# Optimization experiments

Hardware: AMD Instinct MI355X
Metric: run time of the kernel (lower is better)

Reference implementation:

```python
import jax, jax.numpy as jnp
import numpy as np

B, NSM, NLG = 64, 400, 196
SM, LG = 512, 1024
D, H, DH = 4, 16, 64
INNER = H * DH
EPS = 1e-5


def setup_inputs() -> dict:
    key = jax.random.key(0)
    ks = iter(jax.random.split(key, 40))
    def rn(shape, s=0.02):
        return jax.random.normal(next(ks), shape, jnp.float32) * s
    inp = {
        "sm_tokens": rn((B, NSM + 1, SM), 1.0),
        "lg_tokens": rn((B, NLG + 1, LG), 1.0),
    }
    def branch(p, din, dout):
        inp[p + "_pin_w"] = rn((D, din, dout))
        inp[p + "_pin_b"] = jnp.zeros((D, dout), jnp.float32)
        inp[p + "_ng"] = jnp.ones((D, dout), jnp.float32)
        inp[p + "_nb"] = jnp.zeros((D, dout), jnp.float32)
        inp[p + "_wq"] = rn((D, dout, INNER))
        inp[p + "_wkv"] = rn((D, dout, 2 * INNER))
        inp[p + "_wo"] = rn((D, INNER, dout))
        inp[p + "_wob"] = jnp.zeros((D, dout), jnp.float32)
        inp[p + "_pout_w"] = rn((D, dout, din))
        inp[p + "_pout_b"] = jnp.zeros((D, din), jnp.float32)
    branch("a", SM, LG)   # sm_attend_lg: project sm->lg, attention in lg_dim
    branch("b", LG, SM)   # lg_attend_sm: project lg->sm, attention in sm_dim
    return inp


def _attn(cls_tok, ctx, ng, nb, wq, wkv, wo, wob):
    # cls_tok: [B,1,dim]; ctx: [B,S,dim]. Matches lucidrains cross_vit Attention:
    # LayerNorm(x) first; kv context = concat(normed_x, context); context NOT normed.
    scale = DH ** -0.5
    mu = cls_tok.mean(-1, keepdims=True)
    var = ((cls_tok - mu) ** 2).mean(-1, keepdims=True)
    xn = (cls_tok - mu) * jax.lax.rsqrt(var + EPS) * ng + nb
    c = jnp.concatenate([xn, ctx], axis=1)             # kv_include_self=True
    q = (xn @ wq).reshape(B, 1, H, DH)
    k, v = jnp.split(c @ wkv, 2, axis=-1)
    k = k.reshape(B, -1, H, DH)
    v = v.reshape(B, -1, H, DH)
    s = jnp.einsum('bqhd,bkhd->bhqk', q, k) * scale     # [B,H,1,S+1]
    p = jax.nn.softmax(s, axis=-1)
    o = jnp.einsum('bhqk,bkhd->bqhd', p, v).reshape(B, 1, INNER)
    return o @ wo + wob


def _forward(sm_tokens, lg_tokens,
             a_pin_w, a_pin_b, a_ng, a_nb, a_wq, a_wkv, a_wo, a_wob, a_pout_w, a_pout_b,
             b_pin_w, b_pin_b, b_ng, b_nb, b_wq, b_wkv, b_wo, b_wob, b_pout_w, b_pout_b):
    sm_cls, sm_patch = sm_tokens[:, :1], sm_tokens[:, 1:]
    lg_cls, lg_patch = lg_tokens[:, :1], lg_tokens[:, 1:]
    for i in range(D):
        x = sm_cls @ a_pin_w[i] + a_pin_b[i]
        x = _attn(x, lg_patch, a_ng[i], a_nb[i], a_wq[i], a_wkv[i], a_wo[i], a_wob[i])
        sm_cls = x @ a_pout_w[i] + a_pout_b[i] + sm_cls
        y = lg_cls @ b_pin_w[i] + b_pin_b[i]
        y = _attn(y, sm_patch, b_ng[i], b_nb[i], b_wq[i], b_wkv[i], b_wo[i], b_wob[i])
        lg_cls = y @ b_pout_w[i] + b_pout_b[i] + lg_cls
    sm_out = jnp.concatenate([sm_cls, sm_patch], axis=1)
    lg_out = jnp.concatenate([lg_cls, lg_patch], axis=1)
    return sm_out, lg_out


def reference(sm_tokens, lg_tokens,
              a_pin_w, a_pin_b, a_ng, a_nb, a_wq, a_wkv, a_wo, a_wob, a_pout_w, a_pout_b,
              b_pin_w, b_pin_b, b_ng, b_nb, b_wq, b_wkv, b_wo, b_wob, b_pout_w, b_pout_b):
    return _forward(sm_tokens, lg_tokens,
                    a_pin_w, a_pin_b, a_ng, a_nb, a_wq, a_wkv, a_wo, a_wob, a_pout_w, a_pout_b,
                    b_pin_w, b_pin_b, b_ng, b_nb, b_wq, b_wkv, b_wo, b_wob, b_pout_w, b_pout_b)
```

## Files before the change

### kernel.cpp

```cpp
#include <hip/hip_runtime.h>
#include <hip/hip_bf16.h>
#include <math.h>

#define B_     64
#define NSM_   400
#define NLG_   196
#define SM_    512
#define LG_    1024
#define H_     16
#define DH_    64
#define INNER_ 1024
#define SSTR   424
#define PSTR   424

typedef __attribute__((ext_vector_type(8))) short bf16x8;
typedef __attribute__((ext_vector_type(8))) unsigned short u16x8;
typedef __attribute__((ext_vector_type(4))) float f32x4;

__device__ __forceinline__ unsigned short f2b(float f) {
  unsigned u = __float_as_uint(f);
  u = u + 0x7FFFu + ((u >> 16) & 1u);
  return (unsigned short)(u >> 16);
}
__device__ __forceinline__ f32x4 zero4() {
  f32x4 a; a[0] = 0.f; a[1] = 0.f; a[2] = 0.f; a[3] = 0.f; return a;
}


struct CC2 { const float* tok; float* out; unsigned short* abf; float* cls;
             unsigned short* clsb; int Np1, nf4, shift, tot4; };
struct WTDesc { const float* src; unsigned short* dst; unsigned short* dst2; int K, N; };
struct WTArgs { WTDesc d[10]; int cum[11]; };
__global__ __launch_bounds__(256) void setup1(CC2 ca, CC2 cb, WTArgs W, int nw) {
  __shared__ unsigned short tile[64][68];
  const int tid = threadIdx.x;
  if ((int)blockIdx.x < nw) {
    int bx = blockIdx.x, di = 0;
    while (bx >= W.cum[di + 1]) di++;
    int local = bx - W.cum[di];
    WTDesc g = W.d[di];
    int tn = g.N >> 6;
    int tpl = tn * (g.K >> 6);
    int layer = local / tpl, rem = local % tpl;
    int kt = (rem / tn) * 64, nt = (rem % tn) * 64;
    const float* wp = g.src + (size_t)layer * g.K * g.N;
    unsigned short* op = g.dst + (size_t)layer * g.K * g.N;
    unsigned short* d2 = (g.dst2 && nt < 1024)
                             ? g.dst2 + (size_t)layer * g.K * 1024 : nullptr;
#pragma unroll
    for (int p = 0; p < 4; p++) {
      int r = (tid >> 4) + p * 16;
      int c = (tid & 15) * 4;
      const f32x4 v = __builtin_nontemporal_load(
          (const f32x4*)&wp[(size_t)(kt + r) * g.N + nt + c]);
      ushort4 w4;
      w4.x = f2b(v.x); w4.y = f2b(v.y); w4.z = f2b(v.z); w4.w = f2b(v.w);
      *(ushort4*)&tile[r][c] = w4;
      if (d2) *(ushort4*)&d2[(size_t)(kt + r) * 1024 + nt + c] = w4;
    }
    __syncthreads();
    const int r2 = tid >> 2, cseg = tid & 3;
    u16x8 v0, v1;
#pragma unroll
    for (int i = 0; i < 8; i++) v0[i] = tile[cseg * 16 + i][r2];
#pragma unroll
    for (int i = 0; i < 8; i++) v1[i] = tile[cseg * 16 + 8 + i][r2];
    unsigned short* orow = &op[(size_t)(nt + r2) * g.K + kt + cseg * 16];
    *(u16x8*)&orow[0] = v0;
    *(u16x8*)&orow[8] = v1;
  } else {
    const int nblk = gridDim.x - nw;
    const int total = ca.tot4 + cb.tot4;
    for (int i = ((int)blockIdx.x - nw) * 256 + tid; i < total; i += nblk * 256) {
      CC2 g; int idx;
      if (i < ca.tot4) { g = ca; idx = i; } else { g = cb; idx = i - ca.tot4; }
      int rowg = idx >> g.shift, t = idx & ((1 << g.shift) - 1);
      int bb = rowg / g.Np1, row = rowg - bb * g.Np1;
      const f32x4 v = __builtin_nontemporal_load(&((const f32x4*)g.tok)[idx]);
      __builtin_nontemporal_store(v, &((f32x4*)g.out)[idx]);
      ushort4 w2; w2.x = f2b(v.x); w2.y = f2b(v.y); w2.z = f2b(v.z); w2.w = f2b(v.w);
      if (row > 0) {
        ((ushort4*)g.abf)[(size_t)(bb * (g.Np1 - 1) + row - 1) * g.nf4 + t] = w2;
      } else {
        ((f32x4*)g.cls)[(size_t)bb * g.nf4 + t] = v;
        ((ushort4*)g.clsb)[(size_t)bb * g.nf4 + t] = w2;
      }
    }
  }
}

struct TXArgs { const unsigned short* xbf; unsigned short* xT; int Nctx, dout, xstride, nx, ny, nblk; };
__global__ __launch_bounds__(256) void setup2(TXArgs ta, TXArgs tb) {
  __shared__ unsigned short tile[64][68];
  TXArgs g; int bx = blockIdx.x;
  if (bx < ta.nblk) { g = ta; } else { g = tb; bx -= ta.nblk; }
  int cx = bx % g.nx; int rem = bx / g.nx;
  int jy = rem % g.ny; int b = rem / g.ny;
  int jt = jy * 64, ct = cx * 64;
  const int tid = threadIdx.x;
#pragma unroll
  for (int p = 0; p < 4; p++) {
    int row = (tid >> 4) + p * 16;
    int c = (tid & 15) * 4;
    int j = jt + row;
    ushort4 v;
    if (j < g.Nctx) v = *(const ushort4*)&g.xbf[((size_t)b * g.Nctx + j) * g.dout + ct + c];
    else { v.x = 0; v.y = 0; v.z = 0; v.w = 0; }
    *(ushort4*)&tile[row][c] = v;
  }
  __syncthreads();
  const int r2 = tid >> 2, jseg = tid & 3;
  if (jt + jseg * 16 < g.xstride) {
    u16x8 v0, v1;
#pragma unroll
    for (int i = 0; i < 8; i++) v0[i] = tile[jseg * 16 + i][r2];
#pragma unroll
    for (int i = 0; i < 8; i++) v1[i] = tile[jseg * 16 + 8 + i][r2];
    unsigned short* orow = &g.xT[((size_t)b * g.dout + ct + r2) * g.xstride + jt + jseg * 16];
    *(u16x8*)&orow[0] = v0;
    *(u16x8*)&orow[8] = v1;
  }
}

struct SGDesc {
  const unsigned short* A; const unsigned short* WT; const float* bias;
  float* Cf; unsigned short* Cbf; const float* Rf;
  int K, N;
  float* outF; int ostride;
};
struct SGArgs { SGDesc d[4]; int cum[5]; int nd; };
__global__ __launch_bounds__(256) void sg_wide(SGArgs W) {
  int bx = blockIdx.x, di = 0;
  while (di < W.nd - 1 && bx >= W.cum[di + 1]) di++;
  SGDesc g = W.d[di];
  const int n0 = (bx - W.cum[di]) * 16;
  const int tid = threadIdx.x;
  const int lane = tid & 63, mt = tid >> 6;
  const int r16 = lane & 15, kv8 = (lane >> 4) * 8;
  f32x4 acc0 = zero4(), acc1 = zero4();
  const unsigned short* wp = &g.WT[(size_t)(n0 + r16) * g.K + kv8];
  const unsigned short* ap = &g.A[(size_t)(mt * 16 + r16) * g.K + kv8];
  const int K = g.K;
#pragma unroll 2
  for (int k0 = 0; k0 < K; k0 += 64) {
    acc0 = __builtin_amdgcn_mfma_f32_16x16x32_bf16(*(const bf16x8*)&ap[k0],
                                                   *(const bf16x8*)&wp[k0], acc0, 0, 0, 0);
    acc1 = __builtin_amdgcn_mfma_f32_16x16x32_bf16(*(const bf16x8*)&ap[k0 + 32],
                                                   *(const bf16x8*)&wp[k0 + 32], acc1, 0, 0, 0);
  }
  const int rbase = (lane >> 4) * 4;
#pragma unroll
  for (int rr = 0; rr < 4; rr++) {
    int r = mt * 16 + rbase + rr, c = n0 + r16;
    float v = acc0[rr] + acc1[rr];
    if (g.bias) v += g.bias[c];
    if (g.Rf) v += g.Rf[(size_t)r * g.N + c];
    if (g.Cf)  g.Cf[(size_t)r * g.N + c] = v;
    if (g.Cbf) g.Cbf[(size_t)r * g.N + c] = f2b(v);
    if (g.outF) g.outF[(size_t)r * g.ostride + c] = v;
  }
}

struct LNArgs { const float* x; unsigned short* xnb; const float* ng; const float* nb; int dim; };
__global__ __launch_bounds__(256) void ln2(LNArgs la, LNArgs lb) {
  LNArgs g = ((int)blockIdx.x < 64) ? la : lb;
  int b = blockIdx.x & 63, t = threadIdx.x;
  __shared__ float rs[4], rq[4], bc[2];
  const float* xp = g.x + (size_t)b * g.dim;
  float s = 0.f, sq = 0.f;
  for (int c = t; c < g.dim; c += 256) {
    float v = xp[c];
    s += v; sq += v * v;
  }
#pragma unroll
  for (int off = 32; off >= 1; off >>= 1) {
    s += __shfl_down(s, off);
    sq += __shfl_down(sq, off);
  }
  int w = t >> 6;
  if ((t & 63) == 0) { rs[w] = s; rq[w] = sq; }
  __syncthreads();
  if (t == 0) {
    float ts = rs[0] + rs[1] + rs[2] + rs[3];
    float tq = rq[0] + rq[1] + rq[2] + rq[3];
    float mu = ts / g.dim;
    float var = tq / g.dim - mu * mu;
    bc[0] = mu; bc[1] = rsqrtf(var + 1e-5f);
  }
  __syncthreads();
  float mu = bc[0], r = bc[1];
  for (int c = t; c < g.dim; c += 256)
    g.xnb[(size_t)b * g.dim + c] = f2b((xp[c] - mu) * r * g.ng[c] + g.nb[c]);
}

struct QTArgs { const unsigned short* qb16; const unsigned short* wkvnb;
                unsigned short* qt; int dout, ntiles, nblk; };
__global__ __launch_bounds__(256) void qtilde3(QTArgs ga, QTArgs gb) {
  QTArgs g; int bx = blockIdx.x;
  if (bx < ga.nblk) g = ga; else { g = gb; bx -= ga.nblk; }
  const int h = bx / g.ntiles, nt = bx - h * g.ntiles;
  const int n0 = nt * 16;
  const int tid = threadIdx.x, lane = tid & 63, mt = tid >> 6;
  const int r16 = lane & 15, kv8 = (lane >> 4) * 8;
  const unsigned short* ap = g.qb16 + (size_t)(mt * 16 + r16) * INNER_ + h * 64 + kv8;
  const unsigned short* bp = g.wkvnb + (size_t)(n0 + r16) * 1024 + h * 64 + kv8;
  f32x4 acc0 = zero4(), acc1 = zero4();
  acc0 = __builtin_amdgcn_mfma_f32_16x16x32_bf16(*(const bf16x8*)&ap[0],
                                                 *(const bf16x8*)&bp[0], acc0, 0, 0, 0);
  acc1 = __builtin_amdgcn_mfma_f32_16x16x32_bf16(*(const bf16x8*)&ap[32],
                                                 *(const bf16x8*)&bp[32], acc1, 0, 0, 0);
  const int rbase = (lane >> 4) * 4;
#pragma unroll
  for (int rr = 0; rr < 4; rr++) {
    int b = mt * 16 + rbase + rr;
    g.qt[((size_t)b * 16 + h) * g.dout + n0 + r16] = f2b(acc0[rr] + acc1[rr]);
  }
}

struct SArgs { const unsigned short* qt; const unsigned short* xbf; float* S;
               int dout, Nctx, ntj, nbj, nblk; };
__global__ __launch_bounds__(256) void s_gemm(SArgs ga, SArgs gb) {
  SArgs g; int bx;
  if ((int)blockIdx.x < ga.nblk) { g = ga; bx = blockIdx.x; }
  else { g = gb; bx = blockIdx.x - ga.nblk; }
  const int b = bx / g.nbj, jq = bx - b * g.nbj;
  const int tid = threadIdx.x, lane = tid & 63, w = tid >> 6;
  const int jt = jq * 4 + w;
  if (jt >= g.ntj) return;
  const int r16 = lane & 15, kv8 = (lane >> 4) * 8;
  const unsigned short* ap = g.qt + ((size_t)b * 16 + r16) * g.dout + kv8;
  const unsigned short* bp = g.xbf + ((size_t)b * g.Nctx + jt * 16 + r16) * g.dout + kv8;
  f32x4 acc0 = zero4(), acc1 = zero4();
  const int K = g.dout;
#pragma unroll 2
  for (int k0 = 0; k0 < K; k0 += 64) {
    acc0 = __builtin_amdgcn_mfma_f32_16x16x32_bf16(*(const bf16x8*)&ap[k0],
                                                   *(const bf16x8*)&bp[k0], acc0, 0, 0, 0);
    acc1 = __builtin_amdgcn_mfma_f32_16x16x32_bf16(*(const bf16x8*)&ap[k0 + 32],
                                                   *(const bf16x8*)&bp[k0 + 32], acc1, 0, 0, 0);
  }
  const int rbase = (lane >> 4) * 4;
#pragma unroll
  for (int rr = 0; rr < 4; rr++)
    g.S[((size_t)b * 16 + rbase + rr) * SSTR + jt * 16 + r16] = acc0[rr] + acc1[rr];
}

struct SMArgs { const float* S; const float* qb; const float* kvc;
                unsigned short* p; float* pcls; int Nctx, Npad; };
__global__ __launch_bounds__(256) void softmax_p2(SMArgs ga, SMArgs gb) {
  SMArgs g = blockIdx.z ? gb : ga;
  const int h = blockIdx.x, b = blockIdx.y;
  const int t = threadIdx.x;
  __shared__ float red[4], bc;
  float sc = 0.f;
  if (t < 64) sc = g.qb[(size_t)b * INNER_ + h * 64 + t] * g.kvc[(size_t)b * 2048 + h * 64 + t];
#pragma unroll
  for (int o = 32; o >= 1; o >>= 1) sc += __shfl_down(sc, o);
  if (t == 0) bc = sc * 0.125f;
  __syncthreads();
  const float scls = bc;
  const float* Sp = g.S + ((size_t)b * 16 + h) * SSTR;

  float sraw[2] = {-1e30f, -1e30f};
#pragma unroll
  for (int u2 = 0; u2 < 2; u2++) {
    int j = t + u2 * 256;
    if (j < g.Nctx) sraw[u2] = Sp[j] * 0.125f;
  }
  float mx = fmaxf(fmaxf(sraw[0], sraw[1]), scls);
#pragma unroll
  for (int o = 32; o >= 1; o >>= 1) mx = fmaxf(mx, __shfl_down(mx, o));
  if ((t & 63) == 0) red[t >> 6] = mx;
  __syncthreads();
  mx = fmaxf(fmaxf(red[0], red[1]), fmaxf(red[2], red[3]));
  __syncthreads();

  float e0 = (t < g.Nctx) ? expf(sraw[0] - mx) : 0.f;
  float e1 = (t + 256 < g.Nctx) ? expf(sraw[1] - mx) : 0.f;
  float ecls = expf(scls - mx);
  float ls = e0 + e1;
#pragma unroll
  for (int o = 32; o >= 1; o >>= 1) ls += __shfl_down(ls, o);
  if ((t & 63) == 0) red[t >> 6] = ls;
  __syncthreads();
  const float denom = red[0] + red[1] + red[2] + red[3] + ecls;
  const float inv = 1.f / denom;

  unsigned short* pp = g.p + ((size_t)b * 16 + h) * PSTR;
  if (t < g.Nctx) pp[t] = f2b(e0 * inv);
  if (t + 256 < g.Nctx) pp[t + 256] = f2b(e1 * inv);
  for (int j = g.Nctx + t; j < g.Npad; j += 256) pp[j] = 0;
  if (t == 0) g.pcls[b * 16 + h] = ecls * inv;
}

struct UG { const unsigned short* p; const unsigned short* xT; unsigned short* u;
            int dout, Npad, xstride, ntx; };
__global__ __launch_bounds__(256) void ugemm2(UG ga, UG gb) {
  UG g; int bx = blockIdx.x;
  if (bx < ga.ntx) g = ga; else { g = gb; bx -= ga.ntx; }
  const int b = blockIdx.y;
  const int tid = threadIdx.x, lane = tid & 63, w = tid >> 6;
  const int c0 = bx * 64 + w * 16;
  const int r16 = lane & 15, kv8 = (lane >> 4) * 8, rbase = (lane >> 4) * 4;
  const unsigned short* ap = g.p + ((size_t)b * 16 + r16) * PSTR + kv8;
  const unsigned short* bp = g.xT + ((size_t)b * g.dout + c0 + r16) * g.xstride + kv8;
  f32x4 acc0 = zero4(), acc1 = zero4();
  const int Kp = g.Npad;
  int k0 = 0;
  for (; k0 + 64 <= Kp; k0 += 64) {
    acc0 = __builtin_amdgcn_mfma_f32_16x16x32_bf16(*(const bf16x8*)&ap[k0],
                                                   *(const bf16x8*)&bp[k0], acc0, 0, 0, 0);
    acc1 = __builtin_amdgcn_mfma_f32_16x16x32_bf16(*(const bf16x8*)&ap[k0 + 32],
                                                   *(const bf16x8*)&bp[k0 + 32], acc1, 0, 0, 0);
  }
  if (k0 < Kp)
    acc0 = __builtin_amdgcn_mfma_f32_16x16x32_bf16(*(const bf16x8*)&ap[k0],
                                                   *(const bf16x8*)&bp[k0], acc0, 0, 0, 0);
#pragma unroll
  for (int rr = 0; rr < 4; rr++)
    g.u[((size_t)b * 16 + rbase + rr) * g.dout + c0 + r16] = f2b(acc0[rr] + acc1[rr]);
}

struct OArgs {
  const unsigned short* u; const unsigned short* WTkv; const float* kvc; const float* pcls;
  unsigned short* ob; int dout;
};
__global__ __launch_bounds__(256) void ogemm_w(OArgs ga, OArgs gb) {
  OArgs g; int bx = blockIdx.x;
  if (bx < 64) { g = ga; } else { g = gb; bx -= 64; }
  const int h = bx >> 2, dt = bx & 3;
  const int tid = threadIdx.x, lane = tid & 63, mt = tid >> 6;
  const int r16 = lane & 15, kv8 = (lane >> 4) * 8;
  const int dout = g.dout;
  f32x4 acc0 = zero4(), acc1 = zero4();
  const unsigned short* wp = &g.WTkv[(size_t)(1024 + h * 64 + dt * 16 + r16) * dout + kv8];
  const unsigned short* up = &g.u[((size_t)(mt * 16 + r16) * 16 + h) * dout + kv8];
#pragma unroll 2
  for (int k0 = 0; k0 < dout; k0 += 64) {
    acc0 = __builtin_amdgcn_mfma_f32_16x16x32_bf16(*(const bf16x8*)&up[k0],
                                                   *(const bf16x8*)&wp[k0], acc0, 0, 0, 0);
    acc1 = __builtin_amdgcn_mfma_f32_16x16x32_bf16(*(const bf16x8*)&up[k0 + 32],
                                                   *(const bf16x8*)&wp[k0 + 32], acc1, 0, 0, 0);
  }
  const int rbase = (lane >> 4) * 4;
#pragma unroll
  for (int rr = 0; rr < 4; rr++) {
    int bi = mt * 16 + rbase + rr;
    int d = h * 64 + dt * 16 + r16;
    float v = acc0[rr] + acc1[rr] + g.pcls[bi * 16 + h] * g.kvc[(size_t)bi * 2048 + 1024 + d];
    g.ob[(size_t)bi * INNER_ + d] = f2b(v);
  }
}

extern "C" void kernel_launch(void* const* d_in, const int* in_sizes, int n_in,
                              void* d_out, int out_size, void* d_ws, size_t ws_size,
                              hipStream_t stream) {
  const float* sm_tokens = (const float*)d_in[0];
  const float* lg_tokens = (const float*)d_in[1];
  const float* a_pin_w  = (const float*)d_in[2];  const float* a_pin_b  = (const float*)d_in[3];
  const float* a_ng     = (const float*)d_in[4];  const float* a_nb     = (const float*)d_in[5];
  const float* a_wq     = (const float*)d_in[6];  const float* a_wkv    = (const float*)d_in[7];
  const float* a_wo     = (const float*)d_in[8];  const float* a_wob    = (const float*)d_in[9];
  const float* a_pout_w = (const float*)d_in[10]; const float* a_pout_b = (const float*)d_in[11];
  const float* b_pin_w  = (const float*)d_in[12]; const float* b_pin_b  = (const float*)d_in[13];
  const float* b_ng     = (const float*)d_in[14]; const float* b_nb     = (const float*)d_in[15];
  const float* b_wq     = (const float*)d_in[16]; const float* b_wkv    = (const float*)d_in[17];
  const float* b_wo     = (const float*)d_in[18]; const float* b_wob    = (const float*)d_in[19];
  const float* b_pout_w = (const float*)d_in[20]; const float* b_pout_b = (const float*)d_in[21];

  float* out = (float*)d_out;
  char* ws = (char*)d_ws;
  size_t off = 0;
  auto alloc = [&](size_t bytes) -> void* {
    void* pt = ws + off;
    off += (bytes + 255) & ~(size_t)255;
    return pt;
  };
  unsigned short* Abf_lg = (unsigned short*)alloc(((size_t)B_ * NLG_ + 32) * LG_ * 2);
  unsigned short* Abf_sm = (unsigned short*)alloc(((size_t)B_ * NSM_ + 32) * SM_ * 2);
  unsigned short* xT_lg  = (unsigned short*)alloc((size_t)B_ * LG_ * 224 * 2);
  unsigned short* xT_sm  = (unsigned short*)alloc((size_t)B_ * SM_ * 416 * 2);
  unsigned short* WTkv_a = (unsigned short*)alloc((size_t)4 * 2048 * LG_ * 2);
  unsigned short* WTkv_b = (unsigned short*)alloc((size_t)4 * 2048 * SM_ * 2);
  unsigned short* wkvnb_a = (unsigned short*)alloc((size_t)4 * LG_ * 1024 * 2);
  unsigned short* wkvnb_b = (unsigned short*)alloc((size_t)4 * SM_ * 1024 * 2);
  unsigned short* WTpin_a = (unsigned short*)alloc((size_t)4 * SM_ * LG_ * 2);
  unsigned short* WTpin_b = (unsigned short*)alloc((size_t)4 * LG_ * SM_ * 2);
  unsigned short* WTwq_a  = (unsigned short*)alloc((size_t)4 * LG_ * INNER_ * 2);
  unsigned short* WTwq_b  = (unsigned short*)alloc((size_t)4 * SM_ * INNER_ * 2);
  unsigned short* WTwo_a  = (unsigned short*)alloc((size_t)4 * INNER_ * LG_ * 2);
  unsigned short* WTwo_b  = (unsigned short*)alloc((size_t)4 * INNER_ * SM_ * 2);
  unsigned short* WTpout_a = (unsigned short*)alloc((size_t)4 * LG_ * SM_ * 2);
  unsigned short* WTpout_b = (unsigned short*)alloc((size_t)4 * SM_ * LG_ * 2);
  unsigned short* qt_a = (unsigned short*)alloc((size_t)B_ * 16 * LG_ * 2);
  unsigned short* qt_b = (unsigned short*)alloc((size_t)B_ * 16 * SM_ * 2);
  float* S_a = (float*)alloc((size_t)B_ * 16 * SSTR * 4);
  float* S_b = (float*)alloc((size_t)B_ * 16 * SSTR * 4);
  unsigned short* p_a = (unsigned short*)alloc((size_t)B_ * 16 * PSTR * 2);
  unsigned short* p_b = (unsigned short*)alloc((size_t)B_ * 16 * PSTR * 2);
  unsigned short* u_a  = (unsigned short*)alloc((size_t)B_ * 16 * LG_ * 2);
  unsigned short* u_b  = (unsigned short*)alloc((size_t)B_ * 16 * SM_ * 2);
  float* pcls_a = (float*)alloc((size_t)B_ * 16 * 4);
  float* pcls_b = (float*)alloc((size_t)B_ * 16 * 4);
  float* cls_sm = (float*)alloc((size_t)B_ * SM_ * 4);
  float* cls_lg = (float*)alloc((size_t)B_ * LG_ * 4);
  unsigned short* clsb_sm = (unsigned short*)alloc((size_t)B_ * SM_ * 2);
  unsigned short* clsb_lg = (unsigned short*)alloc((size_t)B_ * LG_ * 2);
  float* xbuf_a = (float*)alloc((size_t)B_ * LG_ * 4);
  float* xbuf_b = (float*)alloc((size_t)B_ * SM_ * 4);
  unsigned short* xnb_a = (unsigned short*)alloc((size_t)B_ * LG_ * 2);
  unsigned short* xnb_b = (unsigned short*)alloc((size_t)B_ * SM_ * 2);
  float* qbuf_a = (float*)alloc((size_t)B_ * INNER_ * 4);
  float* qbuf_b = (float*)alloc((size_t)B_ * INNER_ * 4);
  unsigned short* qb16_a = (unsigned short*)alloc((size_t)B_ * INNER_ * 2);
  unsigned short* qb16_b = (unsigned short*)alloc((size_t)B_ * INNER_ * 2);
  float* kvc_a  = (float*)alloc((size_t)B_ * 2048 * 4);
  float* kvc_b  = (float*)alloc((size_t)B_ * 2048 * 4);
  unsigned short* obufb_a = (unsigned short*)alloc((size_t)B_ * INNER_ * 2);
  unsigned short* obufb_b = (unsigned short*)alloc((size_t)B_ * INNER_ * 2);
  unsigned short* t1b_a = (unsigned short*)alloc((size_t)B_ * LG_ * 2);
  unsigned short* t1b_b = (unsigned short*)alloc((size_t)B_ * SM_ * 2);
  (void)ws_size; (void)in_sizes; (void)n_in; (void)out_size;

  const size_t sm_elems = (size_t)B_ * (NSM_ + 1) * SM_;

  CC2 ca{sm_tokens, out, Abf_sm, cls_sm, clsb_sm, NSM_ + 1, SM_ / 4, 7,
         (int)(sm_elems / 4)};
  CC2 cb{lg_tokens, out + sm_elems, Abf_lg, cls_lg, clsb_lg, NLG_ + 1, LG_ / 4, 8,
         (int)((size_t)B_ * (NLG_ + 1) * LG_ / 4)};
  WTArgs W;
  W.d[0] = {a_wkv,    WTkv_a,   wkvnb_a, LG_, 2048};
  W.d[1] = {b_wkv,    WTkv_b,   wkvnb_b, SM_, 2048};
  W.d[2] = {a_pin_w,  WTpin_a,  nullptr, SM_, LG_};
  W.d[3] = {b_pin_w,  WTpin_b,  nullptr, LG_, SM_};
  W.d[4] = {a_wq,     WTwq_a,   nullptr, LG_, INNER_};
  W.d[5] = {b_wq,     WTwq_b,   nullptr, SM_, INNER_};
  W.d[6] = {a_wo,     WTwo_a,   nullptr, INNER_, LG_};
  W.d[7] = {b_wo,     WTwo_b,   nullptr, INNER_, SM_};
  W.d[8] = {a_pout_w, WTpout_a, nullptr, LG_, SM_};
  W.d[9] = {b_pout_w, WTpout_b, nullptr, SM_, LG_};
  W.cum[0] = 0;
  for (int i = 0; i < 10; i++)
    W.cum[i + 1] = W.cum[i] + (W.d[i].K / 64) * (W.d[i].N / 64) * 4;
  setup1<<<W.cum[10] + 2048, 256, 0, stream>>>(ca, cb, W, W.cum[10]);
  TXArgs txa{Abf_lg, xT_lg, NLG_, LG_, 224, LG_ / 64, 4, B_ * (LG_ / 64) * 4};
  TXArgs txb{Abf_sm, xT_sm, NSM_, SM_, 416, SM_ / 64, 7, B_ * (SM_ / 64) * 7};
  setup2<<<txa.nblk + txb.nblk, 256, 0, stream>>>(txa, txb);

  for (int l = 0; l < 4; l++) {
    const unsigned short* WTpin_al = WTpin_a + (size_t)l * SM_ * LG_;
    const unsigned short* WTpin_bl = WTpin_b + (size_t)l * LG_ * SM_;
    const unsigned short* WTwq_al  = WTwq_a  + (size_t)l * LG_ * INNER_;
    const unsigned short* WTwq_bl  = WTwq_b  + (size_t)l * SM_ * INNER_;
    const unsigned short* WTkv_al  = WTkv_a  + (size_t)l * 2048 * LG_;
    const unsigned short* WTkv_bl  = WTkv_b  + (size_t)l * 2048 * SM_;
    const unsigned short* wkvnb_al = wkvnb_a + (size_t)l * LG_ * 1024;
    const unsigned short* wkvnb_bl = wkvnb_b + (size_t)l * SM_ * 1024;
    const unsigned short* WTwo_al  = WTwo_a  + (size_t)l * INNER_ * LG_;
    const unsigned short* WTwo_bl  = WTwo_b  + (size_t)l * INNER_ * SM_;
    const unsigned short* WTpout_al = WTpout_a + (size_t)l * LG_ * SM_;
    const unsigned short* WTpout_bl = WTpout_b + (size_t)l * SM_ * LG_;

    SGArgs Gp; Gp.nd = 2;
    Gp.d[0] = {clsb_sm, WTpin_al, a_pin_b + (size_t)l * LG_, xbuf_a, nullptr, nullptr, SM_, LG_, nullptr, 0};
    Gp.d[1] = {clsb_lg, WTpin_bl, b_pin_b + (size_t)l * SM_, xbuf_b, nullptr, nullptr, LG_, SM_, nullptr, 0};
    Gp.cum[0] = 0; Gp.cum[1] = LG_ / 16; Gp.cum[2] = LG_ / 16 + SM_ / 16;
    sg_wide<<<Gp.cum[2], 256, 0, stream>>>(Gp);
    LNArgs la{xbuf_a, xnb_a, a_ng + (size_t)l * LG_, a_nb + (size_t)l * LG_, LG_};
    LNArgs lb{xbuf_b, xnb_b, b_ng + (size_t)l * SM_, b_nb + (size_t)l * SM_, SM_};
    ln2<<<128, 256, 0, stream>>>(la, lb);
    SGArgs Gq; Gq.nd = 4;
    Gq.d[0] = {xnb_a, WTwq_al, nullptr, qbuf_a, qb16_a, nullptr, LG_, INNER_, nullptr, 0};
    Gq.d[1] = {xnb_a, WTkv_al, nullptr, kvc_a,  nullptr, nullptr, LG_, 2048, nullptr, 0};
    Gq.d[2] = {xnb_b, WTwq_bl, nullptr, qbuf_b, qb16_b, nullptr, SM_, INNER_, nullptr, 0};
    Gq.d[3] = {xnb_b, WTkv_bl, nullptr, kvc_b,  nullptr, nullptr, SM_, 2048, nullptr, 0};
    Gq.cum[0] = 0; Gq.cum[1] = 64; Gq.cum[2] = 192; Gq.cum[3] = 256; Gq.cum[4] = 384;
    sg_wide<<<384, 256, 0, stream>>>(Gq);
    QTArgs qa{qb16_a, wkvnb_al, qt_a, LG_, LG_ / 16, 16 * (LG_ / 16)};
    QTArgs qb{qb16_b, wkvnb_bl, qt_b, SM_, SM_ / 16, 16 * (SM_ / 16)};
    qtilde3<<<qa.nblk + qb.nblk, 256, 0, stream>>>(qa, qb);
    SArgs sa{qt_a, Abf_lg, S_a, LG_, NLG_, 14, 4, B_ * 4};
    SArgs sb{qt_b, Abf_sm, S_b, SM_, NSM_, 26, 7, B_ * 7};
    s_gemm<<<sa.nblk + sb.nblk, 256, 0, stream>>>(sa, sb);
    SMArgs ma{S_a, qbuf_a, kvc_a, p_a, pcls_a, NLG_, 224};
    SMArgs mb{S_b, qbuf_b, kvc_b, p_b, pcls_b, NSM_, 416};
    softmax_p2<<<dim3(H_, B_, 2), 256, 0, stream>>>(ma, mb);
    UG ua{p_a, xT_lg, u_a, LG_, 224, 224, LG_ / 64};
    UG ub{p_b, xT_sm, u_b, SM_, 416, 416, SM_ / 64};
    ugemm2<<<dim3(LG_ / 64 + SM_ / 64, B_), 256, 0, stream>>>(ua, ub);
    OArgs oa{u_a, WTkv_al, kvc_a, pcls_a, obufb_a, LG_};
    OArgs ob{u_b, WTkv_bl, kvc_b, pcls_b, obufb_b, SM_};
    ogemm_w<<<128, 256, 0, stream>>>(oa, ob);
    SGArgs Gw; Gw.nd = 2;
    Gw.d[0] = {obufb_a, WTwo_al, a_wob + (size_t)l * LG_, nullptr, t1b_a, nullptr, INNER_, LG_, nullptr, 0};
    Gw.d[1] = {obufb_b, WTwo_bl, b_wob + (size_t)l * SM_, nullptr, t1b_b, nullptr, INNER_, SM_, nullptr, 0};
    Gw.cum[0] = 0; Gw.cum[1] = LG_ / 16; Gw.cum[2] = LG_ / 16 + SM_ / 16;
    sg_wide<<<Gw.cum[2], 256, 0, stream>>>(Gw);
    float* outF_a = (l == 3) ? out : nullptr;
    float* outF_b = (l == 3) ? out + sm_elems : nullptr;
    SGArgs Gr; Gr.nd = 2;
    Gr.d[0] = {t1b_a, WTpout_al, a_pout_b + (size_t)l * SM_, cls_sm, clsb_sm, cls_sm, LG_, SM_,
               outF_a, (NSM_ + 1) * SM_};
    Gr.d[1] = {t1b_b, WTpout_bl, b_pout_b + (size_t)l * LG_, cls_lg, clsb_lg, cls_lg, SM_, LG_,
               outF_b, (NLG_ + 1) * LG_};
    Gr.cum[0] = 0; Gr.cum[1] = SM_ / 16; Gr.cum[2] = SM_ / 16 + LG_ / 16;
    sg_wide<<<Gr.cum[2], 256, 0, stream>>>(Gr);
  }
}
```

Before: 496.0 us.

## Fuse softmax into score GEMM via last-block atomic counter per batch

Removes the separate softmax kernel launch. Each s_gemm block bumps a per-batch atomic counter after writing its scores, and the last block for that batch runs the softmax over all 16 heads serially. The counters are zeroed in setup1, with a separate counter slice for each layer and branch. This saves one launch per layer, but the 16-head softmax now runs serially inside a single block per batch, which may leave the tail of the kernel poorly parallelised.

```diff
diff --git a/kernel.cpp b/kernel.cpp
--- a/kernel.cpp
+++ b/kernel.cpp
@@ -31,9 +31,10 @@
              unsigned short* clsb; int Np1, nf4, shift, tot4; };
 struct WTDesc { const float* src; unsigned short* dst; unsigned short* dst2; int K, N; };
 struct WTArgs { WTDesc d[10]; int cum[11]; };
-__global__ __launch_bounds__(256) void setup1(CC2 ca, CC2 cb, WTArgs W, int nw) {
+__global__ __launch_bounds__(256) void setup1(CC2 ca, CC2 cb, WTArgs W, int nw, int* cntz) {
   __shared__ unsigned short tile[64][68];
   const int tid = threadIdx.x;
+  if (blockIdx.x == 0 && tid < 512) cntz[tid] = 0;
   if ((int)blockIdx.x < nw) {
     int bx = blockIdx.x, di = 0;
     while (bx >= W.cum[di + 1]) di++;
@@ -218,7 +219,9 @@
 }
 
 struct SArgs { const unsigned short* qt; const unsigned short* xbf; float* S;
-               int dout, Nctx, ntj, nbj, nblk; };
+               const float* qb; const float* kvc; unsigned short* p; float* pcls;
+               int* cnt;
+               int dout, Nctx, Npad, ntj, nbj, nblk; };
 __global__ __launch_bounds__(256) void s_gemm(SArgs ga, SArgs gb) {
   SArgs g; int bx;
   if ((int)blockIdx.x < ga.nblk) { g = ga; bx = blockIdx.x; }
@@ -226,71 +229,72 @@
   const int b = bx / g.nbj, jq = bx - b * g.nbj;
   const int tid = threadIdx.x, lane = tid & 63, w = tid >> 6;
   const int jt = jq * 4 + w;
-  if (jt >= g.ntj) return;
-  const int r16 = lane & 15, kv8 = (lane >> 4) * 8;
-  const unsigned short* ap = g.qt + ((size_t)b * 16 + r16) * g.dout + kv8;
-  const unsigned short* bp = g.xbf + ((size_t)b * g.Nctx + jt * 16 + r16) * g.dout + kv8;
-  f32x4 acc0 = zero4(), acc1 = zero4();
-  const int K = g.dout;
+  if (jt < g.ntj) {
+    const int r16 = lane & 15, kv8 = (lane >> 4) * 8;
+    const unsigned short* ap = g.qt + ((size_t)b * 16 + r16) * g.dout + kv8;
+    const unsigned short* bp = g.xbf + ((size_t)b * g.Nctx + jt * 16 + r16) * g.dout + kv8;
+    f32x4 acc0 = zero4(), acc1 = zero4();
+    const int K = g.dout;
 #pragma unroll 2
-  for (int k0 = 0; k0 < K; k0 += 64) {
-    acc0 = __builtin_amdgcn_mfma_f32_16x16x32_bf16(*(const bf16x8*)&ap[k0],
-                                                   *(const bf16x8*)&bp[k0], acc0, 0, 0, 0);
-    acc1 = __builtin_amdgcn_mfma_f32_16x16x32_bf16(*(const bf16x8*)&ap[k0 + 32],
-                                                   *(const bf16x8*)&bp[k0 + 32], acc1, 0, 0, 0);
-  }
-  const int rbase = (lane >> 4) * 4;
-#pragma unroll
-  for (int rr = 0; rr < 4; rr++)
-    g.S[((size_t)b * 16 + rbase + rr) * SSTR + jt * 16 + r16] = acc0[rr] + acc1[rr];
-}
-
-struct SMArgs { const float* S; const float* qb; const float* kvc;
-                unsigned short* p; float* pcls; int Nctx, Npad; };
-__global__ __launch_bounds__(256) void softmax_p2(SMArgs ga, SMArgs gb) {
-  SMArgs g = blockIdx.z ? gb : ga;
-  const int h = blockIdx.x, b = blockIdx.y;
-  const int t = threadIdx.x;
-  __shared__ float red[4], bc;
-  float sc = 0.f;
-  if (t < 64) sc = g.qb[(size_t)b * INNER_ + h * 64 + t] * g.kvc[(size_t)b * 2048 + h * 64 + t];
-#pragma unroll
-  for (int o = 32; o >= 1; o >>= 1) sc += __shfl_down(sc, o);
-  if (t == 0) bc = sc * 0.125f;
+    for (int k0 = 0; k0 < K; k0 += 64) {
+      acc0 = __builtin_amdgcn_mfma_f32_16x16x32_bf16(*(const bf16x8*)&ap[k0],
+                                                     *(const bf16x8*)&bp[k0], acc0, 0, 0, 0);
+      acc1 = __builtin_amdgcn_mfma_f32_16x16x32_bf16(*(const bf16x8*)&ap[k0 + 32],
+                                                     *(const bf16x8*)&bp[k0 + 32], acc1, 0, 0, 0);
+    }
+    const int rbase = (lane >> 4) * 4;
+#pragma unroll
+    for (int rr = 0; rr < 4; rr++)
+      g.S[((size_t)b * 16 + rbase + rr) * SSTR + jt * 16 + r16] = acc0[rr] + acc1[rr];
+  }
+  __shared__ int lastblk;
+  __shared__ float red[4];
+  __shared__ float bcv;
+  __threadfence();
   __syncthreads();
-  const float scls = bc;
-  const float* Sp = g.S + ((size_t)b * 16 + h) * SSTR;
-
-  float sraw[2] = {-1e30f, -1e30f};
-#pragma unroll
-  for (int u2 = 0; u2 < 2; u2++) {
-    int j = t + u2 * 256;
-    if (j < g.Nctx) sraw[u2] = Sp[j] * 0.125f;
-  }
-  float mx = fmaxf(fmaxf(sraw[0], sraw[1]), scls);
-#pragma unroll
-  for (int o = 32; o >= 1; o >>= 1) mx = fmaxf(mx, __shfl_down(mx, o));
-  if ((t & 63) == 0) red[t >> 6] = mx;
+  if (tid == 0) lastblk = (atomicAdd(&g.cnt[b], 1) == g.nbj - 1) ? 1 : 0;
   __syncthreads();
-  mx = fmaxf(fmaxf(red[0], red[1]), fmaxf(red[2], red[3]));
-  __syncthreads();
-
-  float e0 = (t < g.Nctx) ? expf(sraw[0] - mx) : 0.f;
-  float e1 = (t + 256 < g.Nctx) ? expf(sraw[1] - mx) : 0.f;
-  float ecls = expf(scls - mx);
-  float ls = e0 + e1;
-#pragma unroll
-  for (int o = 32; o >= 1; o >>= 1) ls += __shfl_down(ls, o);
-  if ((t & 63) == 0) red[t >> 6] = ls;
-  __syncthreads();
-  const float denom = red[0] + red[1] + red[2] + red[3] + ecls;
-  const float inv = 1.f / denom;
-
-  unsigned short* pp = g.p + ((size_t)b * 16 + h) * PSTR;
-  if (t < g.Nctx) pp[t] = f2b(e0 * inv);
-  if (t + 256 < g.Nctx) pp[t + 256] = f2b(e1 * inv);
-  for (int j = g.Nctx + t; j < g.Npad; j += 256) pp[j] = 0;
-  if (t == 0) g.pcls[b * 16 + h] = ecls * inv;
+  if (!lastblk) return;
+  __threadfence();
+  for (int h = 0; h < 16; h++) {
+    float sc = 0.f;
+    if (tid < 64) sc = g.qb[(size_t)b * INNER_ + h * 64 + tid] * g.kvc[(size_t)b * 2048 + h * 64 + tid];
+#pragma unroll
+    for (int o = 32; o >= 1; o >>= 1) sc += __shfl_down(sc, o);
+    if (tid == 0) bcv = sc * 0.125f;
+    __syncthreads();
+    const float scls = bcv;
+    const float* Sp = g.S + ((size_t)b * 16 + h) * SSTR;
+    float sraw[2] = {-1e30f, -1e30f};
+#pragma unroll
+    for (int u2 = 0; u2 < 2; u2++) {
+      int j = tid + u2 * 256;
+      if (j < g.Nctx) sraw[u2] = Sp[j] * 0.125f;
+    }
+    float mx = fmaxf(fmaxf(sraw[0], sraw[1]), scls);
+#pragma unroll
+    for (int o = 32; o >= 1; o >>= 1) mx = fmaxf(mx, __shfl_down(mx, o));
+    if ((tid & 63) == 0) red[tid >> 6] = mx;
+    __syncthreads();
+    mx = fmaxf(fmaxf(red[0], red[1]), fmaxf(red[2], red[3]));
+    __syncthreads();
+    float e0 = (tid < g.Nctx) ? expf(sraw[0] - mx) : 0.f;
+    float e1 = (tid + 256 < g.Nctx) ? expf(sraw[1] - mx) : 0.f;
+    float ecls = expf(scls - mx);
+    float ls = e0 + e1;
+#pragma unroll
+    for (int o = 32; o >= 1; o >>= 1) ls += __shfl_down(ls, o);
+    if ((tid & 63) == 0) red[tid >> 6] = ls;
+    __syncthreads();
+    const float denom = red[0] + red[1] + red[2] + red[3] + ecls;
+    const float inv = 1.f / denom;
+    unsigned short* pp = g.p + ((size_t)b * 16 + h) * PSTR;
+    if (tid < g.Nctx) pp[tid] = f2b(e0 * inv);
+    if (tid + 256 < g.Nctx) pp[tid + 256] = f2b(e1 * inv);
+    for (int j = g.Nctx + tid; j < g.Npad; j += 256) pp[j] = 0;
+    if (tid == 0) g.pcls[b * 16 + h] = ecls * inv;
+    __syncthreads();
+  }
 }
 
 struct UG { const unsigned short* p; const unsigned short* xT; unsigned short* u;
@@ -420,6 +424,7 @@
   unsigned short* obufb_b = (unsigned short*)alloc((size_t)B_ * INNER_ * 2);
   unsigned short* t1b_a = (unsigned short*)alloc((size_t)B_ * LG_ * 2);
   unsigned short* t1b_b = (unsigned short*)alloc((size_t)B_ * SM_ * 2);
+  int* cnt = (int*)alloc(512 * sizeof(int));
   (void)ws_size; (void)in_sizes; (void)n_in; (void)out_size;
 
   const size_t sm_elems = (size_t)B_ * (NSM_ + 1) * SM_;
@@ -442,7 +447,7 @@
   W.cum[0] = 0;
   for (int i = 0; i < 10; i++)
     W.cum[i + 1] = W.cum[i] + (W.d[i].K / 64) * (W.d[i].N / 64) * 4;
-  setup1<<<W.cum[10] + 2048, 256, 0, stream>>>(ca, cb, W, W.cum[10]);
+  setup1<<<W.cum[10] + 2048, 256, 0, stream>>>(ca, cb, W, W.cum[10], cnt);
   TXArgs txa{Abf_lg, xT_lg, NLG_, LG_, 224, LG_ / 64, 4, B_ * (LG_ / 64) * 4};
   TXArgs txb{Abf_sm, xT_sm, NSM_, SM_, 416, SM_ / 64, 7, B_ * (SM_ / 64) * 7};
   setup2<<<txa.nblk + txb.nblk, 256, 0, stream>>>(txa, txb);
@@ -479,12 +484,11 @@
     QTArgs qa{qb16_a, wkvnb_al, qt_a, LG_, LG_ / 16, 16 * (LG_ / 16)};
     QTArgs qb{qb16_b, wkvnb_bl, qt_b, SM_, SM_ / 16, 16 * (SM_ / 16)};
     qtilde3<<<qa.nblk + qb.nblk, 256, 0, stream>>>(qa, qb);
-    SArgs sa{qt_a, Abf_lg, S_a, LG_, NLG_, 14, 4, B_ * 4};
-    SArgs sb{qt_b, Abf_sm, S_b, SM_, NSM_, 26, 7, B_ * 7};
+    SArgs sa{qt_a, Abf_lg, S_a, qbuf_a, kvc_a, p_a, pcls_a, cnt + (l * 2 + 0) * 64,
+             LG_, NLG_, 224, 14, 4, B_ * 4};
+    SArgs sb{qt_b, Abf_sm, S_b, qbuf_b, kvc_b, p_b, pcls_b, cnt + (l * 2 + 1) * 64,
+             SM_, NSM_, 416, 26, 7, B_ * 7};
     s_gemm<<<sa.nblk + sb.nblk, 256, 0, stream>>>(sa, sb);
-    SMArgs ma{S_a, qbuf_a, kvc_a, p_a, pcls_a, NLG_, 224};
-    SMArgs mb{S_b, qbuf_b, kvc_b, p_b, pcls_b, NSM_, 416};
-    softmax_p2<<<dim3(H_, B_, 2), 256, 0, stream>>>(ma, mb);
     UG ua{p_a, xT_lg, u_a, LG_, 224, 224, LG_ / 64};
     UG ub{p_b, xT_sm, u_b, SM_, 416, 416, SM_ / 64};
     ugemm2<<<dim3(LG_ / 64 + SM_ / 64, B_), 256, 0, stream>>>(ua, ub);
```

Result: slower. 925.1 us (+86.5%).
